# Kernel tuning notes

Hardware: AMD Instinct MI355X
Metric: run time of the kernel (lower is better)

## Reference

```python
import jax, jax.numpy as jnp
import numpy as np

B, S, D, H, DFF, K = 16, 1024, 1024, 16, 4096, 3


def setup_inputs() -> dict:
    key = jax.random.key(0)
    ks = jax.random.split(key, 8)
    f = lambda k, sh: jax.random.normal(k, sh, jnp.float32) * 0.02
    return dict(
        x=jax.random.normal(ks[0], (B, S, D), jnp.float32),
        mask=jnp.ones((B, 1, S), jnp.int32),
        alpha1=jnp.ones((D,), jnp.float32), bias1=jnp.zeros((D,), jnp.float32),
        alpha2=jnp.ones((D,), jnp.float32), bias2=jnp.zeros((D,), jnp.float32),
        W_l1=f(ks[1], (D, 2 * D)), b_l1=jnp.zeros((2 * D,), jnp.float32),
        conv_w=f(ks[2], (H, K)),
        W_l2=f(ks[3], (D, D)), b_l2=jnp.zeros((D,), jnp.float32),
        W_ff1=f(ks[4], (D, DFF)), b_ff1=jnp.zeros((DFF,), jnp.float32),
        W_ff2=f(ks[5], (DFF, D)), b_ff2=jnp.zeros((D,), jnp.float32),
    )


def _norm(x, alpha, bias, eps=1e-6):
    # Norm: alpha * (x - mean) / (std + eps) + bias, torch std is unbiased (ddof=1)
    mu = x.mean(-1, keepdims=True)
    sd = x.std(-1, keepdims=True, ddof=1)
    return alpha * (x - mu) / (sd + eps) + bias


def _lightconv(x, conv_w):
    # x: [B, S, C]; conv_w: [H, K] softmax-normalized over K; channels in a head share kernel
    C = x.shape[-1]
    w = jax.nn.softmax(conv_w, axis=-1)              # [H, K]
    wk = jnp.repeat(w, C // H, axis=0)[:, None, :]   # [C, 1, K] depthwise kernel
    y = jax.lax.conv_general_dilated(
        x.transpose(0, 2, 1), wk, (1,), [(K // 2, (K - 1) // 2)],
        dimension_numbers=('NCH', 'OIH', 'NCH'), feature_group_count=C)
    return y.transpose(0, 2, 1)


def reference(x, mask, alpha1, bias1, alpha2, bias2, W_l1, b_l1, conv_w,
              W_l2, b_l2, W_ff1, b_ff1, W_ff2, b_ff2):
    # --- lightweight-conv sublayer ---
    res = x
    h = _norm(x, alpha1, bias1)
    h = h @ W_l1 + b_l1                         # [B,S,2C]
    a, b = jnp.split(h, 2, axis=-1)
    h = a * jax.nn.sigmoid(b)                   # GLU -> [B,S,C]
    cm = mask[:, -1, :][:, :, None]             # [B,S,1]
    h = jnp.where(cm == 0, 0.0, h)
    h = _lightconv(h, conv_w)
    h = h @ W_l2 + b_l2
    x = res + h
    # --- FFN sublayer ---
    res = x
    h = _norm(x, alpha2, bias2)
    h = jax.nn.relu(h @ W_ff1 + b_ff1) @ W_ff2 + b_ff2
    return res + h
```

## Files before the change

### kernel.cpp

```cpp
#include <hip/hip_runtime.h>

typedef unsigned short ushort_t;
typedef __attribute__((ext_vector_type(8))) short s8v;
typedef __attribute__((ext_vector_type(4))) float f4v;

__device__ __forceinline__ float b2f(ushort_t h) {
    union { unsigned u; float f; } c; c.u = ((unsigned)h) << 16; return c.f;
}
__device__ __forceinline__ ushort_t f2b(float f) {
    union { float f; unsigned u; } c; c.f = f;
    unsigned u = c.u;
    return (ushort_t)((u + 0x7fffu + ((u >> 16) & 1u)) >> 16);
}

__device__ __forceinline__ void glds16(const void* g, void* l) {
    __builtin_amdgcn_global_load_lds(
        (const __attribute__((address_space(1))) void*)g,
        (__attribute__((address_space(3))) void*)l, 16, 0, 0);
}

template <int PERM>
__global__ __launch_bounds__(256) void trans_k(const float* __restrict__ W,
                                               ushort_t* __restrict__ Wt,
                                               int K, int N) {
    __shared__ float tile[64][65];
    int k0 = blockIdx.x * 64, n0 = blockIdx.y * 64;
    int t = threadIdx.x;
    int c = t & 63, r4 = t >> 6;
#pragma unroll
    for (int i = 0; i < 16; ++i) {
        int r = i * 4 + r4;
        tile[r][c] = W[(size_t)(k0 + r) * N + n0 + c];
    }
    __syncthreads();
#pragma unroll
    for (int i = 0; i < 16; ++i) {
        int r = i * 4 + r4;
        int s = n0 + r;
        int d;
        if (PERM) {
            int a = (s < 1024);
            int s2 = a ? s : s - 1024;
            d = ((s2 >> 7) << 8) + (a ? 0 : 128) + (s2 & 127);
        } else {
            d = s;
        }
        Wt[(size_t)d * K + k0 + c] = f2b(tile[c][r]);
    }
}

__global__ __launch_bounds__(256) void norm_k(const float* __restrict__ x,
                                              const float* __restrict__ al,
                                              const float* __restrict__ be,
                                              ushort_t* __restrict__ out) {
    int row = blockIdx.x;
    const float4* xr = (const float4*)(x + (size_t)row * 1024);
    float4 v = xr[threadIdx.x];
    float s = v.x + v.y + v.z + v.w;
    float q = v.x * v.x + v.y * v.y + v.z * v.z + v.w * v.w;
#pragma unroll
    for (int o = 32; o > 0; o >>= 1) {
        s += __shfl_down(s, o);
        q += __shfl_down(q, o);
    }
    __shared__ float ss[4], qq[4];
    int lane = threadIdx.x & 63, wv = threadIdx.x >> 6;
    if (lane == 0) { ss[wv] = s; qq[wv] = q; }
    __syncthreads();
    s = ss[0] + ss[1] + ss[2] + ss[3];
    q = qq[0] + qq[1] + qq[2] + qq[3];
    float mu = s * (1.f / 1024.f);
    float var = (q - 1024.f * mu * mu) * (1.f / 1023.f);
    var = fmaxf(var, 0.f);
    float inv = 1.f / (sqrtf(var) + 1e-6f);
    float4 a4 = ((const float4*)al)[threadIdx.x];
    float4 b4 = ((const float4*)be)[threadIdx.x];
    ushort4 o4;
    o4.x = f2b(a4.x * (v.x - mu) * inv + b4.x);
    o4.y = f2b(a4.y * (v.y - mu) * inv + b4.y);
    o4.z = f2b(a4.z * (v.z - mu) * inv + b4.z);
    o4.w = f2b(a4.w * (v.w - mu) * inv + b4.w);
    ((ushort4*)(out + (size_t)row * 1024))[threadIdx.x] = o4;
}

__global__ __launch_bounds__(256) void conv_k(const ushort_t* __restrict__ g,
                                              const float* __restrict__ cw,
                                              ushort_t* __restrict__ out) {
    int i = blockIdx.x * 256 + threadIdx.x;
    int row = i >> 7;
    int cc = (i & 127) << 3;
    int s = row & 1023;
    int head = cc >> 6;
    float w0 = cw[head * 3 + 0], w1 = cw[head * 3 + 1], w2 = cw[head * 3 + 2];
    float mx = fmaxf(w0, fmaxf(w1, w2));
    float e0 = __expf(w0 - mx), e1 = __expf(w1 - mx), e2 = __expf(w2 - mx);
    float inv = 1.f / (e0 + e1 + e2);
    w0 = e0 * inv; w1 = e1 * inv; w2 = e2 * inv;
    size_t base = (size_t)row * 1024 + cc;
    s8v z = {0, 0, 0, 0, 0, 0, 0, 0};
    s8v vm = (s > 0)    ? *(const s8v*)(g + base - 1024) : z;
    s8v v0 = *(const s8v*)(g + base);
    s8v vp = (s < 1023) ? *(const s8v*)(g + base + 1024) : z;
    s8v ov;
#pragma unroll
    for (int j = 0; j < 8; ++j) {
        float r = w0 * b2f((ushort_t)vm[j]) + w1 * b2f((ushort_t)v0[j]) +
                  w2 * b2f((ushort_t)vp[j]);
        ov[j] = (short)f2b(r);
    }
    *(s8v*)(out + base) = ov;
}

template <int EPI>
__global__ __launch_bounds__(512, 1) void gemm_k(const ushort_t* __restrict__ A,
                                                 const ushort_t* __restrict__ Bt,
                                                 const float* __restrict__ bias,
                                                 const int* __restrict__ maskp,
                                                 const float* res, float* outf,
                                                 ushort_t* outb, int N, int K) {
    __shared__ char smem[131072] __attribute__((aligned(128)));
    const int NBN = N >> 8;
    const int nwg = gridDim.x;
    const int per = nwg >> 3;
    const int tt = (blockIdx.x & 7) * per + (blockIdx.x >> 3);
    const int gw = NBN << 3;
    const int g = tt / gw;
    const int rem = tt - g * gw;
    const int bm = (g << 3) + (rem & 7);
    const int bn = rem >> 3;

    const int t = threadIdx.x;
    const int l = t & 63, w = t >> 6;
    const int wm = w >> 2, wn = w & 3;
    const int lr = l & 15, lk = l >> 4;

    const int swzel = (((t & 3) ^ ((t >> 3) & 3)) << 3);
    const int r0 = t >> 2;
    const ushort_t* pA0 = A + (size_t)(bm * 256 + r0) * K + swzel;
    const ushort_t* pA1 = pA0 + (size_t)128 * K;
    const ushort_t* pB0 = Bt + (size_t)(bn * 256 + r0) * K + swzel;
    const ushort_t* pB1 = pB0 + (size_t)128 * K;

    const int fswz = ((lk ^ ((lr >> 1) & 3)) << 4);
    int aoff[8], boff[4];
#pragma unroll
    for (int m = 0; m < 8; ++m)
        aoff[m] = (wm * 128 + m * 16 + lr) * 64 + fswz;
#pragma unroll
    for (int n = 0; n < 4; ++n)
        boff[n] = 16384 + (wn * 64 + n * 16 + lr) * 64 + fswz;

    f4v acc[8][4];
#pragma unroll
    for (int m = 0; m < 8; ++m)
#pragma unroll
        for (int n = 0; n < 4; ++n) acc[m][n] = f4v{0.f, 0.f, 0.f, 0.f};

    const int NK = K >> 5;

#pragma unroll
    for (int p = 0; p < 3; ++p) {
        char* d = smem + p * 32768 + t * 16;
        glds16(pA0 + p * 32, d);
        glds16(pA1 + p * 32, d + 8192);
        glds16(pB0 + p * 32, d + 16384);
        glds16(pB1 + p * 32, d + 24576);
    }
    asm volatile("s_waitcnt vmcnt(8)");
    __builtin_amdgcn_s_barrier();
    __builtin_amdgcn_sched_barrier(0);

    s8v aL0[4], bF0[4], aL1[4], bF1[4], aH[4];
#pragma unroll
    for (int m = 0; m < 4; ++m) aL0[m] = *(const s8v*)(smem + aoff[m]);
#pragma unroll
    for (int n = 0; n < 4; ++n) bF0[n] = *(const s8v*)(smem + boff[n]);

#define KSTEP(I, CAL, CBF, NAL, NBF)                                           \
    {                                                                          \
        const int i_ = (I);                                                    \
        const char* cb_ = smem + (size_t)(i_ & 3) * 32768;                     \
        const char* nb_ = smem + (size_t)((i_ + 1) & 3) * 32768;               \
        int st_ = i_ + 3; if (st_ >= NK) st_ = NK - 1;                         \
        char* sd_ = smem + (size_t)((i_ + 3) & 3) * 32768 + t * 16;            \
        const int ko_ = st_ * 32;                                              \
                 \
        _Pragma("unroll")                                                      \
        for (int m = 0; m < 4; ++m) aH[m] = *(const s8v*)(cb_ + aoff[4 + m]);  \
        glds16(pA0 + ko_, sd_);                                                \
        glds16(pA1 + ko_, sd_ + 8192);                                         \
        glds16(pB0 + ko_, sd_ + 16384);                                        \
        glds16(pB1 + ko_, sd_ + 24576);                                        \
        __builtin_amdgcn_s_setprio(1);                                         \
        _Pragma("unroll")                                                      \
        for (int m = 0; m < 4; ++m)                                            \
            _Pragma("unroll")                                                  \
            for (int n = 0; n < 4; ++n)                                        \
                acc[m][n] = __builtin_amdgcn_mfma_f32_16x16x32_bf16(           \
                    CAL[m], CBF[n], acc[m][n], 0, 0, 0);                       \
        __builtin_amdgcn_s_setprio(0);                                         \
        __builtin_amdgcn_sched_barrier(0);                                     \
        asm volatile("s_waitcnt vmcnt(6)");               \
        __builtin_amdgcn_s_barrier();                                          \
        __builtin_amdgcn_sched_barrier(0);                                     \
           \
        _Pragma("unroll")                                                      \
        for (int m = 0; m < 4; ++m) NAL[m] = *(const s8v*)(nb_ + aoff[m]);     \
        _Pragma("unroll")                                                      \
        for (int n = 0; n < 4; ++n) NBF[n] = *(const s8v*)(nb_ + boff[n]);     \
        __builtin_amdgcn_s_setprio(1);                                         \
        _Pragma("unroll")                                                      \
        for (int m = 0; m < 4; ++m)                                            \
            _Pragma("unroll")                                                  \
            for (int n = 0; n < 4; ++n)                                        \
                acc[4 + m][n] = __builtin_amdgcn_mfma_f32_16x16x32_bf16(       \
                    aH[m], CBF[n], acc[4 + m][n], 0, 0, 0);                    \
        __builtin_amdgcn_s_setprio(0);                                         \
    }

    for (int ii = 0; ii < NK; ii += 2) {
        KSTEP(ii, aL0, bF0, aL1, bF1);
        KSTEP(ii + 1, aL1, bF1, aL0, bF0);
    }
#undef KSTEP

    if (EPI == 1) {
#pragma unroll
        for (int n = 0; n < 4; ++n) {
            int gcol = bn * 256 + wn * 64 + n * 16 + lr;
            float bb = bias[gcol];
#pragma unroll
            for (int m = 0; m < 8; ++m) {
#pragma unroll
                for (int r = 0; r < 4; ++r) {
                    int grow = bm * 256 + wm * 128 + m * 16 + lk * 4 + r;
                    size_t oi = (size_t)grow * N + gcol;
                    outf[oi] = acc[m][n][r] + bb + res[oi];
                }
            }
        }
    } else {
        asm volatile("s_waitcnt vmcnt(0)" ::: "memory");
        __builtin_amdgcn_s_barrier();
        float bb4[4];
#pragma unroll
        for (int n = 0; n < 4; ++n) {
            int d = bn * 256 + wn * 64 + n * 16 + lr;
            int src = d;
            if (EPI == 3)
                src = ((d >> 8) << 7) + (d & 127) + (((d >> 7) & 1) << 10);
            bb4[n] = bias[src];
        }
#pragma unroll
        for (int m = 0; m < 8; ++m)
#pragma unroll
            for (int n = 0; n < 4; ++n)
#pragma unroll
                for (int r = 0; r < 4; ++r) {
                    int row = wm * 128 + m * 16 + lk * 4 + r;
                    int colb = ((wn * 64 + n * 16 + lr) * 2) ^ ((row & 3) << 4);
                    float v = acc[m][n][r] + bb4[n];
                    if (EPI == 2) v = fmaxf(v, 0.f);
                    *(ushort_t*)(smem + row * 512 + colb) = f2b(v);
                }
        __builtin_amdgcn_s_barrier();
        if (EPI == 3) {
#pragma unroll
            for (int s = 0; s < 8; ++s) {
                int row = s * 32 + (t >> 4);
                int abyt = row * 512 + (((t & 15) * 16) ^ ((row & 3) << 4));
                s8v av = *(const s8v*)(smem + abyt);
                s8v bv = *(const s8v*)(smem + abyt + 256);
                int grow = bm * 256 + row;
                float mval =
                    (maskp[(grow >> 10) * 1024 + (grow & 1023)] == 0) ? 0.f : 1.f;
                s8v ov;
#pragma unroll
                for (int j = 0; j < 8; ++j) {
                    float a = b2f((ushort_t)av[j]);
                    float xx = b2f((ushort_t)bv[j]);
                    ov[j] = (short)f2b(a * mval / (1.f + __expf(-xx)));
                }
                *(s8v*)(outb + (size_t)grow * (N >> 1) + bn * 128 +
                        (t & 15) * 8) = ov;
            }
        } else {
#pragma unroll
            for (int s = 0; s < 16; ++s) {
                int row = s * 16 + (t >> 5);
                int byt = row * 512 + (((t & 31) * 16) ^ ((row & 3) << 4));
                int grow = bm * 256 + row;
                int gcol = bn * 256 + (t & 31) * 8;
                *(s8v*)(outb + (size_t)grow * N + gcol) =
                    *(const s8v*)(smem + byt);
            }
        }
    }
}

extern "C" void kernel_launch(void* const* d_in, const int* in_sizes, int n_in,
                              void* d_out, int out_size, void* d_ws, size_t ws_size,
                              hipStream_t stream) {
    const float* x      = (const float*)d_in[0];
    const int*   mask   = (const int*)d_in[1];
    const float* alpha1 = (const float*)d_in[2];
    const float* bias1  = (const float*)d_in[3];
    const float* alpha2 = (const float*)d_in[4];
    const float* bias2  = (const float*)d_in[5];
    const float* W_l1   = (const float*)d_in[6];
    const float* b_l1   = (const float*)d_in[7];
    const float* conv_w = (const float*)d_in[8];
    const float* W_l2   = (const float*)d_in[9];
    const float* b_l2   = (const float*)d_in[10];
    const float* W_ff1  = (const float*)d_in[11];
    const float* b_ff1  = (const float*)d_in[12];
    const float* W_ff2  = (const float*)d_in[13];
    const float* b_ff2  = (const float*)d_in[14];
    float* out = (float*)d_out;

    char* ws = (char*)d_ws;
    size_t off = 0;
    auto alloc = [&](size_t b) {
        char* p = ws + off;
        off += (b + 255) & ~(size_t)255;
        return p;
    };
    ushort_t* Wl1t  = (ushort_t*)alloc(2048ull * 1024 * 2);
    ushort_t* Wl2t  = (ushort_t*)alloc(1024ull * 1024 * 2);
    ushort_t* Wff1t = (ushort_t*)alloc(4096ull * 1024 * 2);
    ushort_t* Wff2t = (ushort_t*)alloc(1024ull * 4096 * 2);
    char* regA = alloc(134217728ull);
    ushort_t* B1 = (ushort_t*)alloc(33554432ull);
    ushort_t* C1 = (ushort_t*)alloc(33554432ull);
    ushort_t* G1 = (ushort_t*)regA;
    ushort_t* f1 = (ushort_t*)regA;

    const int R = 16384;

    trans_k<1><<<dim3(16, 32), 256, 0, stream>>>(W_l1, Wl1t, 1024, 2048);
    trans_k<0><<<dim3(16, 16), 256, 0, stream>>>(W_l2, Wl2t, 1024, 1024);
    trans_k<0><<<dim3(16, 64), 256, 0, stream>>>(W_ff1, Wff1t, 1024, 4096);
    trans_k<0><<<dim3(64, 16), 256, 0, stream>>>(W_ff2, Wff2t, 4096, 1024);

    norm_k<<<R, 256, 0, stream>>>(x, alpha1, bias1, B1);
    gemm_k<3><<<64 * 8, 512, 0, stream>>>(B1, Wl1t, b_l1, mask, nullptr,
                                          nullptr, G1, 2048, 1024);
    conv_k<<<8192, 256, 0, stream>>>(G1, conv_w, C1);
    gemm_k<1><<<64 * 4, 512, 0, stream>>>(C1, Wl2t, b_l2, nullptr, x, out,
                                          nullptr, 1024, 1024);

    norm_k<<<R, 256, 0, stream>>>(out, alpha2, bias2, B1);
    gemm_k<2><<<64 * 16, 512, 0, stream>>>(B1, Wff1t, b_ff1, nullptr, nullptr,
                                           nullptr, f1, 4096, 1024);
    gemm_k<1><<<64 * 4, 512, 0, stream>>>(f1, Wff2t, b_ff2, nullptr, out, out,
                                          nullptr, 1024, 4096);
}
```

Before: 549.0 us.

## Add 4-wave 256x256 GEMM kernel with 128x128 per-wave tiles for FFN layers

Adds a new GEMM kernel using 256 threads (4 waves), each computing a 128x128 sub-tile with an 8x8 accumulator array, and uses it for both FFN GEMMs. The main loop becomes simpler: one K step per iteration, loading all fragments and then issuing 64 MFMAs. Each wave reuses more data from LDS per fragment load and has fewer barriers per unit of work. The cost is very high register pressure (256 accumulator VGPRs plus fragments), a risk of spills, and less latency hiding from having fewer waves. The original gemm_k is specialised to the GLU epilogue only.

```diff
diff --git a/kernel.cpp b/kernel.cpp
--- a/kernel.cpp
+++ b/kernel.cpp
@@ -120,8 +120,7 @@
                                                  ushort_t* outb, int N, int K) {
     __shared__ char smem[131072] __attribute__((aligned(128)));
     const int NBN = N >> 8;
-    const int nwg = gridDim.x;
-    const int per = nwg >> 3;
+    const int per = gridDim.x >> 3;
     const int tt = (blockIdx.x & 7) * per + (blockIdx.x >> 3);
     const int gw = NBN << 3;
     const int g = tt / gw;
@@ -184,7 +183,6 @@
         int st_ = i_ + 3; if (st_ >= NK) st_ = NK - 1;                         \
         char* sd_ = smem + (size_t)((i_ + 3) & 3) * 32768 + t * 16;            \
         const int ko_ = st_ * 32;                                              \
-                 \
         _Pragma("unroll")                                                      \
         for (int m = 0; m < 4; ++m) aH[m] = *(const s8v*)(cb_ + aoff[4 + m]);  \
         glds16(pA0 + ko_, sd_);                                                \
@@ -200,10 +198,9 @@
                     CAL[m], CBF[n], acc[m][n], 0, 0, 0);                       \
         __builtin_amdgcn_s_setprio(0);                                         \
         __builtin_amdgcn_sched_barrier(0);                                     \
-        asm volatile("s_waitcnt vmcnt(6)");               \
+        asm volatile("s_waitcnt vmcnt(6)");                                    \
         __builtin_amdgcn_s_barrier();                                          \
         __builtin_amdgcn_sched_barrier(0);                                     \
-           \
         _Pragma("unroll")                                                      \
         for (int m = 0; m < 4; ++m) NAL[m] = *(const s8v*)(nb_ + aoff[m]);     \
         _Pragma("unroll")                                                      \
@@ -246,9 +243,7 @@
 #pragma unroll
         for (int n = 0; n < 4; ++n) {
             int d = bn * 256 + wn * 64 + n * 16 + lr;
-            int src = d;
-            if (EPI == 3)
-                src = ((d >> 8) << 7) + (d & 127) + (((d >> 7) & 1) << 10);
+            int src = ((d >> 8) << 7) + (d & 127) + (((d >> 7) & 1) << 10);
             bb4[n] = bias[src];
         }
 #pragma unroll
@@ -259,41 +254,164 @@
                 for (int r = 0; r < 4; ++r) {
                     int row = wm * 128 + m * 16 + lk * 4 + r;
                     int colb = ((wn * 64 + n * 16 + lr) * 2) ^ ((row & 3) << 4);
-                    float v = acc[m][n][r] + bb4[n];
-                    if (EPI == 2) v = fmaxf(v, 0.f);
-                    *(ushort_t*)(smem + row * 512 + colb) = f2b(v);
+                    *(ushort_t*)(smem + row * 512 + colb) =
+                        f2b(acc[m][n][r] + bb4[n]);
                 }
         __builtin_amdgcn_s_barrier();
-        if (EPI == 3) {
-#pragma unroll
-            for (int s = 0; s < 8; ++s) {
-                int row = s * 32 + (t >> 4);
-                int abyt = row * 512 + (((t & 15) * 16) ^ ((row & 3) << 4));
-                s8v av = *(const s8v*)(smem + abyt);
-                s8v bv = *(const s8v*)(smem + abyt + 256);
-                int grow = bm * 256 + row;
-                float mval =
-                    (maskp[(grow >> 10) * 1024 + (grow & 1023)] == 0) ? 0.f : 1.f;
-                s8v ov;
-#pragma unroll
-                for (int j = 0; j < 8; ++j) {
-                    float a = b2f((ushort_t)av[j]);
-                    float xx = b2f((ushort_t)bv[j]);
-                    ov[j] = (short)f2b(a * mval / (1.f + __expf(-xx)));
+#pragma unroll
+        for (int s = 0; s < 8; ++s) {
+            int row = s * 32 + (t >> 4);
+            int abyt = row * 512 + (((t & 15) * 16) ^ ((row & 3) << 4));
+            s8v av = *(const s8v*)(smem + abyt);
+            s8v bv = *(const s8v*)(smem + abyt + 256);
+            int grow = bm * 256 + row;
+            float mval = (maskp[grow] == 0) ? 0.f : 1.f;
+            s8v ov;
+#pragma unroll
+            for (int j = 0; j < 8; ++j) {
+                float a = b2f((ushort_t)av[j]);
+                float xx = b2f((ushort_t)bv[j]);
+                ov[j] = (short)f2b(a * mval / (1.f + __expf(-xx)));
+            }
+            *(s8v*)(outb + (size_t)grow * (N >> 1) + bn * 128 + (t & 15) * 8) =
+                ov;
+        }
+    }
+}
+
+template <int EPI>
+__global__ __launch_bounds__(256, 1) void gemm4w_k(
+    const ushort_t* __restrict__ A, const ushort_t* __restrict__ Bt,
+    const float* __restrict__ bias, const float* res, float* outf,
+    ushort_t* outb, int N, int K) {
+    __shared__ char smem[131072] __attribute__((aligned(128)));
+    const int NBN = N >> 8;
+    const int per = gridDim.x >> 3;
+    const int tt = (blockIdx.x & 7) * per + (blockIdx.x >> 3);
+    const int gw = NBN << 3;
+    const int g = tt / gw;
+    const int rem = tt - g * gw;
+    const int bm = (g << 3) + (rem & 7);
+    const int bn = rem >> 3;
+
+    const int t = threadIdx.x;
+    const int l = t & 63, w = t >> 6;
+    const int wm = w >> 1, wn = w & 1;
+    const int lr = l & 15, lk = l >> 4;
+
+    const int swzel = (((t & 3) ^ ((t >> 3) & 3)) << 3);
+    const int r0 = t >> 2;
+    const ushort_t* pA[4];
+    const ushort_t* pB[4];
+#pragma unroll
+    for (int j = 0; j < 4; ++j) {
+        pA[j] = A + (size_t)(bm * 256 + r0 + 64 * j) * K + swzel;
+        pB[j] = Bt + (size_t)(bn * 256 + r0 + 64 * j) * K + swzel;
+    }
+
+    const int fswz = ((lk ^ ((lr >> 1) & 3)) << 4);
+    int aoff[8], boff[8];
+#pragma unroll
+    for (int m = 0; m < 8; ++m) {
+        aoff[m] = (wm * 128 + m * 16 + lr) * 64 + fswz;
+        boff[m] = 16384 + (wn * 128 + m * 16 + lr) * 64 + fswz;
+    }
+
+    f4v acc[8][8];
+#pragma unroll
+    for (int m = 0; m < 8; ++m)
+#pragma unroll
+        for (int n = 0; n < 8; ++n) acc[m][n] = f4v{0.f, 0.f, 0.f, 0.f};
+
+    const int NK = K >> 5;
+
+#pragma unroll
+    for (int p = 0; p < 3; ++p) {
+        char* d = smem + p * 32768 + t * 16;
+#pragma unroll
+        for (int j = 0; j < 4; ++j) {
+            glds16(pA[j] + p * 32, d + j * 4096);
+            glds16(pB[j] + p * 32, d + 16384 + j * 4096);
+        }
+    }
+    asm volatile("s_waitcnt vmcnt(16)");
+    __builtin_amdgcn_s_barrier();
+    __builtin_amdgcn_sched_barrier(0);
+
+    for (int i = 0; i < NK; ++i) {
+        const char* cb = smem + (size_t)(i & 3) * 32768;
+        int st = i + 3; if (st >= NK) st = NK - 1;
+        const int ko = st * 32;
+        char* sd = smem + (size_t)((i + 3) & 3) * 32768 + t * 16;
+
+#pragma unroll
+        for (int j = 0; j < 4; ++j) {
+            glds16(pA[j] + ko, sd + j * 4096);
+            glds16(pB[j] + ko, sd + 16384 + j * 4096);
+        }
+
+        s8v aF[8], bF[8];
+#pragma unroll
+        for (int m = 0; m < 8; ++m) aF[m] = *(const s8v*)(cb + aoff[m]);
+#pragma unroll
+        for (int n = 0; n < 8; ++n) bF[n] = *(const s8v*)(cb + boff[n]);
+        __builtin_amdgcn_s_setprio(1);
+#pragma unroll
+        for (int m = 0; m < 8; ++m)
+#pragma unroll
+            for (int n = 0; n < 8; ++n)
+                acc[m][n] = __builtin_amdgcn_mfma_f32_16x16x32_bf16(
+                    aF[m], bF[n], acc[m][n], 0, 0, 0);
+        __builtin_amdgcn_s_setprio(0);
+
+        __builtin_amdgcn_sched_barrier(0);
+        asm volatile("s_waitcnt vmcnt(16)");
+        __builtin_amdgcn_s_barrier();
+        __builtin_amdgcn_sched_barrier(0);
+    }
+
+    if (EPI == 1) {
+#pragma unroll
+        for (int n = 0; n < 8; ++n) {
+            int gcol = bn * 256 + wn * 128 + n * 16 + lr;
+            float bb = bias[gcol];
+#pragma unroll
+            for (int m = 0; m < 8; ++m) {
+#pragma unroll
+                for (int r = 0; r < 4; ++r) {
+                    int grow = bm * 256 + wm * 128 + m * 16 + lk * 4 + r;
+                    size_t oi = (size_t)grow * N + gcol;
+                    outf[oi] = acc[m][n][r] + bb + res[oi];
                 }
-                *(s8v*)(outb + (size_t)grow * (N >> 1) + bn * 128 +
-                        (t & 15) * 8) = ov;
             }
-        } else {
-#pragma unroll
-            for (int s = 0; s < 16; ++s) {
-                int row = s * 16 + (t >> 5);
-                int byt = row * 512 + (((t & 31) * 16) ^ ((row & 3) << 4));
-                int grow = bm * 256 + row;
-                int gcol = bn * 256 + (t & 31) * 8;
-                *(s8v*)(outb + (size_t)grow * N + gcol) =
-                    *(const s8v*)(smem + byt);
-            }
+        }
+    } else {
+        asm volatile("s_waitcnt vmcnt(0)" ::: "memory");
+        __builtin_amdgcn_s_barrier();
+        float bb8[8];
+#pragma unroll
+        for (int n = 0; n < 8; ++n)
+            bb8[n] = bias[bn * 256 + wn * 128 + n * 16 + lr];
+#pragma unroll
+        for (int m = 0; m < 8; ++m)
+#pragma unroll
+            for (int n = 0; n < 8; ++n)
+#pragma unroll
+                for (int r = 0; r < 4; ++r) {
+                    int row = wm * 128 + m * 16 + lk * 4 + r;
+                    int colb =
+                        ((wn * 128 + n * 16 + lr) * 2) ^ ((row & 3) << 4);
+                    *(ushort_t*)(smem + row * 512 + colb) =
+                        f2b(fmaxf(acc[m][n][r] + bb8[n], 0.f));
+                }
+        __builtin_amdgcn_s_barrier();
+#pragma unroll
+        for (int s = 0; s < 32; ++s) {
+            int row = s * 8 + (t >> 5);
+            int byt = row * 512 + (((t & 31) * 16) ^ ((row & 3) << 4));
+            int grow = bm * 256 + row;
+            int gcol = bn * 256 + (t & 31) * 8;
+            *(s8v*)(outb + (size_t)grow * N + gcol) = *(const s8v*)(smem + byt);
         }
     }
 }
@@ -350,8 +468,8 @@
                                           nullptr, 1024, 1024);
 
     norm_k<<<R, 256, 0, stream>>>(out, alpha2, bias2, B1);
-    gemm_k<2><<<64 * 16, 512, 0, stream>>>(B1, Wff1t, b_ff1, nullptr, nullptr,
-                                           nullptr, f1, 4096, 1024);
-    gemm_k<1><<<64 * 4, 512, 0, stream>>>(f1, Wff2t, b_ff2, nullptr, out, out,
-                                          nullptr, 1024, 4096);
-}
+    gemm4w_k<2><<<64 * 16, 256, 0, stream>>>(B1, Wff1t, b_ff1, nullptr,
+                                             nullptr, f1, 4096, 1024);
+    gemm4w_k<1><<<64 * 4, 256, 0, stream>>>(f1, Wff2t, b_ff2, out, out,
+                                            nullptr, 1024, 4096);
+}
```

Measured after the change: 609.2 us. +11.0%, slower.
